# Optimization experiments

Measured on AMD Instinct MI355X. Metric: run time of the kernel, lower is better.

The kernel has to match this reference:

```python
import jax, jax.numpy as jnp
import numpy as np

C = 1024
RANK = 8


def _layernorm(x, g, b, eps=1e-5):
    mu = jnp.mean(x, axis=-1, keepdims=True)
    var = jnp.var(x, axis=-1, keepdims=True)
    return (x - mu) * jax.lax.rsqrt(var + eps) * g + b


def setup_inputs() -> dict:
    key = jax.random.key(0)
    ks = jax.random.split(key, 10)
    B, T = 4, 4096
    x = jax.random.normal(ks[0], (B, T, C), dtype=jnp.float32)
    # parameters (match torch inits)
    W0 = jnp.eye(C, dtype=jnp.float32) * 0.1
    A_init = jax.random.normal(ks[1], (C, RANK), dtype=jnp.float32) * 0.01
    B_init = jnp.zeros((RANK, C), dtype=jnp.float32)
    log_lr = jnp.full((C,), float(np.log(0.1)), dtype=jnp.float32)
    s = 1.0 / np.sqrt(C)
    Wq = jax.random.uniform(ks[2], (C, C), minval=-s, maxval=s, dtype=jnp.float32)
    Wk = jax.random.uniform(ks[3], (C, C), minval=-s, maxval=s, dtype=jnp.float32)
    Wv = jax.random.uniform(ks[4], (C, C), minval=-s, maxval=s, dtype=jnp.float32)
    Wo = jax.random.uniform(ks[5], (C, C), minval=-s, maxval=s, dtype=jnp.float32)
    Wg = jax.random.uniform(ks[6], (C, C), minval=-s, maxval=s, dtype=jnp.float32)
    ln_g = jnp.ones((C,), dtype=jnp.float32)
    ln_b = jnp.zeros((C,), dtype=jnp.float32)
    ls_g = jnp.full((C,), 1e-4, dtype=jnp.float32)  # LayerScale gamma
    return {"x": x, "W0": W0, "A_init": A_init, "B_init": B_init,
            "log_lr": log_lr, "Wq": Wq, "Wk": Wk, "Wv": Wv, "Wo": Wo,
            "Wg": Wg, "ln_g": ln_g, "ln_b": ln_b, "ls_g": ls_g}


def reference(x, W0, A_init, B_init, log_lr, Wq, Wk, Wv, Wo, Wg, ln_g, ln_b, ls_g):
    B, T, _ = x.shape
    h = _layernorm(x, ln_g, ln_b)
    # dual-form TTT (training path: q/k/v projections, full K @ W0)
    Q = jnp.einsum('btc,dc->btd', h, Wq)
    K = jnp.einsum('btc,dc->btd', h, Wk)
    V = jnp.einsum('btc,dc->btd', h, Wv)
    lr = jnp.minimum(jnp.exp(log_lr), 1.0)  # clamp(max=1.0)
    y0 = jnp.einsum('btc,cd->btd', K, W0) + jnp.einsum('btr,rd->btd', jnp.einsum('btc,cr->btr', K, A_init), B_init)
    error = y0 - V
    loss = jnp.mean(error ** 2)
    gradient = K * error                     # [B,T,C]
    grad_cumsum = jnp.cumsum(gradient, axis=1)
    grad_shift = jnp.concatenate([jnp.zeros((B, 1, gradient.shape[-1]), gradient.dtype), grad_cumsum[:, :-1, :]], axis=1)
    correction = Q * lr[None, None, :] * grad_shift
    pos = jnp.arange(1, T + 1, dtype=correction.dtype)
    pos_scale = (1.0 / (1.0 + 0.1 * jnp.log(pos)))[None, :, None]
    out = y0 - correction * pos_scale
    # gate, out projection, layer scale, residual
    gate = jax.nn.sigmoid(jnp.einsum('btc,dc->btd', x, Wg))
    out = out * gate
    out = jnp.einsum('btc,dc->btd', out, Wo) * ls_g
    return (x + out, loss)
```

## Files before the change

kernel.cpp:

```cpp
#include <hip/hip_runtime.h>
#include <stdint.h>
#include <math.h>

typedef unsigned short u16;
typedef __attribute__((ext_vector_type(8))) short short8;
typedef __attribute__((ext_vector_type(4))) float f32x4;

__device__ __forceinline__ float bf2f(u16 u){
  union { unsigned int i; float f; } v; v.i = ((unsigned int)u) << 16; return v.f;
}
__device__ __forceinline__ u16 f2bf(float f){
  union { float f; unsigned int i; } v; v.f = f;
  return (u16)((v.i + 0x7FFFu + ((v.i >> 16) & 1u)) >> 16);
}

__global__ void ln_prep(const float* __restrict__ x, const float* __restrict__ g,
                        const float* __restrict__ bta, u16* __restrict__ h,
                        u16* __restrict__ xb, float* __restrict__ loss){
  if (blockIdx.x == 0 && threadIdx.x == 0) loss[0] = 0.f;
  int row = blockIdx.x, tid = threadIdx.x;
  const float4* xr = (const float4*)(x + (size_t)row * 1024);
  float4 v = xr[tid];
  float s  = v.x + v.y + v.z + v.w;
  float s2 = v.x*v.x + v.y*v.y + v.z*v.z + v.w*v.w;
  #pragma unroll
  for (int o = 32; o > 0; o >>= 1){ s += __shfl_down(s, o); s2 += __shfl_down(s2, o); }
  __shared__ float red[8];
  if ((tid & 63) == 0){ red[tid >> 6] = s; red[4 + (tid >> 6)] = s2; }
  __syncthreads();
  float ts = red[0]+red[1]+red[2]+red[3];
  float t2 = red[4]+red[5]+red[6]+red[7];
  float mu   = ts * (1.0f/1024.0f);
  float var  = t2 * (1.0f/1024.0f) - mu*mu;
  float rstd = rsqrtf(var + 1e-5f);
  float4 gg = ((const float4*)g)[tid];
  float4 bb = ((const float4*)bta)[tid];
  ushort4 hv, xv;
  hv.x = f2bf((v.x-mu)*rstd*gg.x + bb.x);
  hv.y = f2bf((v.y-mu)*rstd*gg.y + bb.y);
  hv.z = f2bf((v.z-mu)*rstd*gg.z + bb.z);
  hv.w = f2bf((v.w-mu)*rstd*gg.w + bb.w);
  xv.x = f2bf(v.x); xv.y = f2bf(v.y); xv.z = f2bf(v.z); xv.w = f2bf(v.w);
  ((ushort4*)h )[(size_t)row*256 + tid] = hv;
  ((ushort4*)xb)[(size_t)row*256 + tid] = xv;
}

__global__ void conv5(const float* __restrict__ a, const float* __restrict__ b,
                      const float* __restrict__ c, const float* __restrict__ d,
                      const float* __restrict__ e,
                      u16* oa, u16* ob, u16* oc, u16* od, u16* oe){
  int sel = blockIdx.y;
  const float* s = sel==0?a : sel==1?b : sel==2?c : sel==3?d : e;
  u16* o = sel==0?oa : sel==1?ob : sel==2?oc : sel==3?od : oe;
  int i = blockIdx.x*256 + threadIdx.x;
  float4 v = ((const float4*)s)[i];
  ushort4 r; r.x=f2bf(v.x); r.y=f2bf(v.y); r.z=f2bf(v.z); r.w=f2bf(v.w);
  ((ushort4*)o)[i] = r;
}

__global__ void weff_k(const float* __restrict__ W0, const float* __restrict__ Ai,
                       const float* __restrict__ Bi, u16* __restrict__ Wet){
  __shared__ float tile[32][33];
  int d0 = blockIdx.x*32, e0 = blockIdx.y*32;
  int tid = threadIdx.x;
  int lr = tid >> 5, lc = tid & 31;
  #pragma unroll
  for (int s = 0; s < 4; ++s){
    int e = e0 + s*8 + lr, d = d0 + lc;
    float v = W0[(size_t)e*1024 + d];
    #pragma unroll
    for (int r = 0; r < 8; ++r) v += Ai[e*8 + r] * Bi[(size_t)r*1024 + d];
    tile[s*8 + lr][lc] = v;
  }
  __syncthreads();
  #pragma unroll
  for (int s = 0; s < 4; ++s){
    int d = d0 + s*8 + lr, e = e0 + lc;
    Wet[(size_t)d*1024 + e] = f2bf(tile[lc][s*8 + lr]);
  }
}

template<int EPI>
__device__ __forceinline__ void gemm_body(const u16* __restrict__ A, const u16* __restrict__ Bm,
    u16* __restrict__ Cb, float* __restrict__ Cf, const float* __restrict__ lsg,
    const float* __restrict__ xres, int mblk, int nblk){
  __shared__ u16 As[128*64];
  __shared__ u16 Bs[128*64];
  const int tid  = threadIdx.x;
  const int lane = tid & 63;
  const int w    = tid >> 6;
  const int m0 = mblk * 128, n0 = nblk * 128;
  const int lrow = lane >> 3, lcol8 = (lane & 7) * 8;
  const int wm = w & 1, wn = w >> 1;
  const int l15 = lane & 15, quad = lane >> 4;

  f32x4 acc[4][4] = {};

  #pragma unroll 1
  for (int kk = 0; kk < 1024; kk += 64){
    #pragma unroll
    for (int it = 0; it < 4; ++it){
      int r0 = w*8 + it*32;
      const u16* ga = A  + (size_t)(m0 + r0 + lrow)*1024 + kk + lcol8;
      __builtin_amdgcn_global_load_lds((const __attribute__((address_space(1))) unsigned int*)ga,
          (__attribute__((address_space(3))) unsigned int*)(As + r0*64), 16, 0, 0);
      const u16* gb = Bm + (size_t)(n0 + r0 + lrow)*1024 + kk + lcol8;
      __builtin_amdgcn_global_load_lds((const __attribute__((address_space(1))) unsigned int*)gb,
          (__attribute__((address_space(3))) unsigned int*)(Bs + r0*64), 16, 0, 0);
    }
    __syncthreads();
    #pragma unroll
    for (int kh = 0; kh < 2; ++kh){
      int kb = kh*32 + quad*8;
      short8 af[4], bfv[4];
      #pragma unroll
      for (int i = 0; i < 4; ++i) af[i]  = *(const short8*)(As + (wm*64 + i*16 + l15)*64 + kb);
      #pragma unroll
      for (int j = 0; j < 4; ++j) bfv[j] = *(const short8*)(Bs + (wn*64 + j*16 + l15)*64 + kb);
      #pragma unroll
      for (int i = 0; i < 4; ++i)
        #pragma unroll
        for (int j = 0; j < 4; ++j)
          acc[i][j] = __builtin_amdgcn_mfma_f32_16x16x32_bf16(af[i], bfv[j], acc[i][j], 0, 0, 0);
    }
    __syncthreads();
  }

  const int rbase = quad * 4;
  if (EPI == 0){
    #pragma unroll
    for (int i = 0; i < 4; ++i){
      int row = m0 + wm*64 + i*16 + rbase;
      #pragma unroll
      for (int j = 0; j < 4; ++j){
        int col = n0 + wn*64 + j*16 + l15;
        #pragma unroll
        for (int r = 0; r < 4; ++r)
          Cb[(size_t)(row + r)*1024 + col] = f2bf(acc[i][j][r]);
      }
    }
  } else {
    float lsv[4];
    #pragma unroll
    for (int j = 0; j < 4; ++j) lsv[j] = lsg[n0 + wn*64 + j*16 + l15];
    #pragma unroll
    for (int i = 0; i < 4; ++i){
      int row = m0 + wm*64 + i*16 + rbase;
      #pragma unroll
      for (int j = 0; j < 4; ++j){
        int col = n0 + wn*64 + j*16 + l15;
        #pragma unroll
        for (int r = 0; r < 4; ++r){
          size_t idx = (size_t)(row + r)*1024 + col;
          Cf[idx] = acc[i][j][r] * lsv[j] + xres[idx];
        }
      }
    }
  }
}

__global__ void gemm_qkvg(const u16* __restrict__ h, const u16* __restrict__ xb,
                          const u16* __restrict__ Wqb, const u16* __restrict__ Wkb,
                          const u16* __restrict__ Wvb, const u16* __restrict__ Wgb,
                          u16* __restrict__ Qb, u16* __restrict__ Kb,
                          u16* __restrict__ Vb, u16* __restrict__ Gb){
  int sel = blockIdx.y >> 3;
  const u16* A  = (sel == 3) ? xb : h;
  const u16* Bm = sel==0?Wqb : sel==1?Wkb : sel==2?Wvb : Wgb;
  u16* Out      = sel==0?Qb  : sel==1?Kb  : sel==2?Vb  : Gb;
  gemm_body<0>(A, Bm, Out, nullptr, nullptr, nullptr, blockIdx.x, blockIdx.y & 7);
}

__global__ void gemm_plain(const u16* __restrict__ A, const u16* __restrict__ Bm,
                           u16* __restrict__ C){
  gemm_body<0>(A, Bm, C, nullptr, nullptr, nullptr, blockIdx.x, blockIdx.y);
}

__global__ void gemm_final(const u16* __restrict__ A, const u16* __restrict__ Bm,
                           float* __restrict__ C, const float* __restrict__ lsg,
                           const float* __restrict__ xres){
  gemm_body<1>(A, Bm, nullptr, C, lsg, xres, blockIdx.x, blockIdx.y);
}

__global__ void scan1(const u16* __restrict__ Kb, const u16* __restrict__ Vb,
                      const u16* __restrict__ Yb, float* __restrict__ part,
                      float* __restrict__ loss){
  int tid = threadIdx.x;
  int c = blockIdx.x*256 + tid;
  int ch = blockIdx.y, b = blockIdx.z;
  size_t base = ((size_t)b*4096 + (size_t)ch*128)*1024 + c;
  float g = 0.f, ls = 0.f;
  #pragma unroll 8
  for (int t = 0; t < 128; ++t){
    size_t idx = base + (size_t)t*1024;
    float kv = bf2f(Kb[idx]), vv = bf2f(Vb[idx]), yv = bf2f(Yb[idx]);
    float e = yv - vv;
    g += kv*e; ls += e*e;
  }
  part[((size_t)(b*32 + ch))*1024 + c] = g;
  #pragma unroll
  for (int o = 32; o > 0; o >>= 1) ls += __shfl_down(ls, o);
  __shared__ float red[4];
  if ((tid & 63) == 0) red[tid >> 6] = ls;
  __syncthreads();
  if (tid == 0) atomicAdd(loss, red[0]+red[1]+red[2]+red[3]);
}

__global__ void scan2(const u16* __restrict__ Kb, const u16* __restrict__ Vb,
                      const u16* __restrict__ Yb, const u16* __restrict__ Qb,
                      const u16* __restrict__ Gb, const float* __restrict__ part,
                      const float* __restrict__ llr, u16* __restrict__ OutPre){
  int tid = threadIdx.x;
  int c = blockIdx.x*256 + tid;
  int ch = blockIdx.y, b = blockIdx.z;
  float run = 0.f;
  for (int j = 0; j < ch; ++j) run += part[((size_t)(b*32 + j))*1024 + c];
  float lrc = fminf(expf(llr[c]), 1.0f);
  size_t base = ((size_t)b*4096 + (size_t)ch*128)*1024 + c;
  #pragma unroll 4
  for (int t = 0; t < 128; ++t){
    size_t idx = base + (size_t)t*1024;
    float kv = bf2f(Kb[idx]), vv = bf2f(Vb[idx]), yv = bf2f(Yb[idx]);
    float qv = bf2f(Qb[idx]), gl = bf2f(Gb[idx]);
    float e = yv - vv;
    int tg = ch*128 + t + 1;
    float ps = 1.0f/(1.0f + 0.1f*logf((float)tg));
    float gate = 1.0f/(1.0f + expf(-gl));
    float o = (yv - qv*lrc*run*ps) * gate;
    OutPre[idx] = f2bf(o);
    run += kv*e;
  }
}

__global__ void finloss(const float* __restrict__ loss, float* __restrict__ o){
  o[0] = loss[0] * (1.0f/16777216.0f);
}

extern "C" void kernel_launch(void* const* d_in, const int* in_sizes, int n_in,
                              void* d_out, int out_size, void* d_ws, size_t ws_size,
                              hipStream_t stream){
  const float* x   = (const float*)d_in[0];
  const float* W0  = (const float*)d_in[1];
  const float* Ai  = (const float*)d_in[2];
  const float* Bi  = (const float*)d_in[3];
  const float* llr = (const float*)d_in[4];
  const float* Wq  = (const float*)d_in[5];
  const float* Wk  = (const float*)d_in[6];
  const float* Wv  = (const float*)d_in[7];
  const float* Wo  = (const float*)d_in[8];
  const float* Wg  = (const float*)d_in[9];
  const float* lng = (const float*)d_in[10];
  const float* lnb = (const float*)d_in[11];
  const float* lsg = (const float*)d_in[12];
  float* out = (float*)d_out;

  const size_t TOK = 16384, CC = 1024;
  char* p = (char*)d_ws;
  float* loss = (float*)p; p += 256;
  u16* h   = (u16*)p; p += TOK*CC*2;
  u16* xb  = (u16*)p; p += TOK*CC*2;
  u16* Qb  = (u16*)p; p += TOK*CC*2;
  u16* Kb  = (u16*)p; p += TOK*CC*2;
  u16* Vb  = (u16*)p; p += TOK*CC*2;
  u16* Gb  = (u16*)p; p += TOK*CC*2;
  u16* Wqb = (u16*)p; p += CC*CC*2;
  u16* Wkb = (u16*)p; p += CC*CC*2;
  u16* Wvb = (u16*)p; p += CC*CC*2;
  u16* Wgb = (u16*)p; p += CC*CC*2;
  u16* Wob = (u16*)p; p += CC*CC*2;
  u16* Wet = (u16*)p; p += CC*CC*2;
  float* part = (float*)p; p += (size_t)4*32*1024*4;

  ln_prep<<<16384, 256, 0, stream>>>(x, lng, lnb, h, xb, loss);
  conv5<<<dim3(1024, 5), 256, 0, stream>>>(Wq, Wk, Wv, Wg, Wo, Wqb, Wkb, Wvb, Wgb, Wob);
  weff_k<<<dim3(32, 32), 256, 0, stream>>>(W0, Ai, Bi, Wet);
  gemm_qkvg<<<dim3(128, 32), 256, 0, stream>>>(h, xb, Wqb, Wkb, Wvb, Wgb, Qb, Kb, Vb, Gb);
  gemm_plain<<<dim3(128, 8), 256, 0, stream>>>(Kb, Wet, h);
  scan1<<<dim3(4, 32, 4), 256, 0, stream>>>(Kb, Vb, h, part, loss);
  scan2<<<dim3(4, 32, 4), 256, 0, stream>>>(Kb, Vb, h, Qb, Gb, part, llr, Qb);
  gemm_final<<<dim3(128, 8), 256, 0, stream>>>(Qb, Wob, out, lsg, x);
  finloss<<<1, 1, 0, stream>>>(loss, out + 16777216);
}
```

Measured before the change: 468.8 us.

## Fuse gradient chunk-sum and loss into y0 GEMM epilogue; swizzle LDS tiles

```diff
diff --git a/kernel.cpp b/kernel.cpp
--- a/kernel.cpp
+++ b/kernel.cpp
@@ -83,16 +83,21 @@
 template<int EPI>
 __device__ __forceinline__ void gemm_body(const u16* __restrict__ A, const u16* __restrict__ Bm,
     u16* __restrict__ Cb, float* __restrict__ Cf, const float* __restrict__ lsg,
-    const float* __restrict__ xres, int mblk, int nblk){
+    const float* __restrict__ xres,
+    const u16* __restrict__ Kb2, const u16* __restrict__ Vb2,
+    u16* __restrict__ Gr, float* __restrict__ part, float* __restrict__ loss,
+    int mblk, int nblk){
   __shared__ u16 As[128*64];
   __shared__ u16 Bs[128*64];
   const int tid  = threadIdx.x;
   const int lane = tid & 63;
   const int w    = tid >> 6;
   const int m0 = mblk * 128, n0 = nblk * 128;
-  const int lrow = lane >> 3, lcol8 = (lane & 7) * 8;
+  const int lrow = lane >> 3;
+  const int gcol8 = (((lane & 7) ^ (lrow & 7)) * 8);
   const int wm = w & 1, wn = w >> 1;
   const int l15 = lane & 15, quad = lane >> 4;
+  const int sw  = (l15 & 7);
 
   f32x4 acc[4][4] = {};
 
@@ -101,22 +106,23 @@
     #pragma unroll
     for (int it = 0; it < 4; ++it){
       int r0 = w*8 + it*32;
-      const u16* ga = A  + (size_t)(m0 + r0 + lrow)*1024 + kk + lcol8;
+      const u16* ga = A  + (size_t)(m0 + r0 + lrow)*1024 + kk + gcol8;
       __builtin_amdgcn_global_load_lds((const __attribute__((address_space(1))) unsigned int*)ga,
           (__attribute__((address_space(3))) unsigned int*)(As + r0*64), 16, 0, 0);
-      const u16* gb = Bm + (size_t)(n0 + r0 + lrow)*1024 + kk + lcol8;
+      const u16* gb = Bm + (size_t)(n0 + r0 + lrow)*1024 + kk + gcol8;
       __builtin_amdgcn_global_load_lds((const __attribute__((address_space(1))) unsigned int*)gb,
           (__attribute__((address_space(3))) unsigned int*)(Bs + r0*64), 16, 0, 0);
     }
     __syncthreads();
     #pragma unroll
     for (int kh = 0; kh < 2; ++kh){
-      int kb = kh*32 + quad*8;
+      int kbi = kh*4 + quad;
+      int koff = ((kbi ^ sw) * 8);
       short8 af[4], bfv[4];
       #pragma unroll
-      for (int i = 0; i < 4; ++i) af[i]  = *(const short8*)(As + (wm*64 + i*16 + l15)*64 + kb);
-      #pragma unroll
-      for (int j = 0; j < 4; ++j) bfv[j] = *(const short8*)(Bs + (wn*64 + j*16 + l15)*64 + kb);
+      for (int i = 0; i < 4; ++i) af[i]  = *(const short8*)(As + (wm*64 + i*16 + l15)*64 + koff);
+      #pragma unroll
+      for (int j = 0; j < 4; ++j) bfv[j] = *(const short8*)(Bs + (wn*64 + j*16 + l15)*64 + koff);
       #pragma unroll
       for (int i = 0; i < 4; ++i)
         #pragma unroll
@@ -139,7 +145,7 @@
           Cb[(size_t)(row + r)*1024 + col] = f2bf(acc[i][j][r]);
       }
     }
-  } else {
+  } else if (EPI == 1){
     float lsv[4];
     #pragma unroll
     for (int j = 0; j < 4; ++j) lsv[j] = lsg[n0 + wn*64 + j*16 + l15];
@@ -156,6 +162,41 @@
         }
       }
     }
+  } else {
+    float csum[4] = {0.f, 0.f, 0.f, 0.f};
+    float ls = 0.f;
+    #pragma unroll
+    for (int i = 0; i < 4; ++i){
+      int row = m0 + wm*64 + i*16 + rbase;
+      #pragma unroll
+      for (int j = 0; j < 4; ++j){
+        int col = n0 + wn*64 + j*16 + l15;
+        #pragma unroll
+        for (int r = 0; r < 4; ++r){
+          size_t idx = (size_t)(row + r)*1024 + col;
+          float y  = acc[i][j][r];
+          float kv = bf2f(Kb2[idx]);
+          float vv = bf2f(Vb2[idx]);
+          float e  = y - vv;
+          float gv = kv * e;
+          Cb[idx] = f2bf(y);
+          Gr[idx] = f2bf(gv);
+          csum[j] += gv;
+          ls += e * e;
+        }
+      }
+    }
+    float* colred = (float*)As;
+    if (tid < 132) colred[tid] = 0.f;
+    __syncthreads();
+    #pragma unroll
+    for (int j = 0; j < 4; ++j) atomicAdd(&colred[wn*64 + j*16 + l15], csum[j]);
+    #pragma unroll
+    for (int o = 32; o > 0; o >>= 1) ls += __shfl_down(ls, o);
+    if (lane == 0) atomicAdd(&colred[128 + w], ls);
+    __syncthreads();
+    if (tid < 128) part[(size_t)mblk * 1024 + n0 + tid] = colred[tid];
+    if (tid == 0) atomicAdd(loss, colred[128]+colred[129]+colred[130]+colred[131]);
   }
 }
 
@@ -168,48 +209,29 @@
   const u16* A  = (sel == 3) ? xb : h;
   const u16* Bm = sel==0?Wqb : sel==1?Wkb : sel==2?Wvb : Wgb;
   u16* Out      = sel==0?Qb  : sel==1?Kb  : sel==2?Vb  : Gb;
-  gemm_body<0>(A, Bm, Out, nullptr, nullptr, nullptr, blockIdx.x, blockIdx.y & 7);
-}
-
-__global__ void gemm_plain(const u16* __restrict__ A, const u16* __restrict__ Bm,
-                           u16* __restrict__ C){
-  gemm_body<0>(A, Bm, C, nullptr, nullptr, nullptr, blockIdx.x, blockIdx.y);
+  gemm_body<0>(A, Bm, Out, nullptr, nullptr, nullptr,
+               nullptr, nullptr, nullptr, nullptr, nullptr, blockIdx.x, blockIdx.y & 7);
+}
+
+__global__ void gemm_y0(const u16* __restrict__ Kb, const u16* __restrict__ Wet,
+                        u16* __restrict__ Yb, const u16* __restrict__ Vb,
+                        u16* __restrict__ Gr, float* __restrict__ part,
+                        float* __restrict__ loss){
+  gemm_body<2>(Kb, Wet, Yb, nullptr, nullptr, nullptr,
+               Kb, Vb, Gr, part, loss, blockIdx.x, blockIdx.y);
 }
 
 __global__ void gemm_final(const u16* __restrict__ A, const u16* __restrict__ Bm,
                            float* __restrict__ C, const float* __restrict__ lsg,
                            const float* __restrict__ xres){
-  gemm_body<1>(A, Bm, nullptr, C, lsg, xres, blockIdx.x, blockIdx.y);
-}
-
-__global__ void scan1(const u16* __restrict__ Kb, const u16* __restrict__ Vb,
-                      const u16* __restrict__ Yb, float* __restrict__ part,
-                      float* __restrict__ loss){
-  int tid = threadIdx.x;
-  int c = blockIdx.x*256 + tid;
-  int ch = blockIdx.y, b = blockIdx.z;
-  size_t base = ((size_t)b*4096 + (size_t)ch*128)*1024 + c;
-  float g = 0.f, ls = 0.f;
-  #pragma unroll 8
-  for (int t = 0; t < 128; ++t){
-    size_t idx = base + (size_t)t*1024;
-    float kv = bf2f(Kb[idx]), vv = bf2f(Vb[idx]), yv = bf2f(Yb[idx]);
-    float e = yv - vv;
-    g += kv*e; ls += e*e;
-  }
-  part[((size_t)(b*32 + ch))*1024 + c] = g;
-  #pragma unroll
-  for (int o = 32; o > 0; o >>= 1) ls += __shfl_down(ls, o);
-  __shared__ float red[4];
-  if ((tid & 63) == 0) red[tid >> 6] = ls;
-  __syncthreads();
-  if (tid == 0) atomicAdd(loss, red[0]+red[1]+red[2]+red[3]);
-}
-
-__global__ void scan2(const u16* __restrict__ Kb, const u16* __restrict__ Vb,
-                      const u16* __restrict__ Yb, const u16* __restrict__ Qb,
-                      const u16* __restrict__ Gb, const float* __restrict__ part,
-                      const float* __restrict__ llr, u16* __restrict__ OutPre){
+  gemm_body<1>(A, Bm, nullptr, C, lsg, xres,
+               nullptr, nullptr, nullptr, nullptr, nullptr, blockIdx.x, blockIdx.y);
+}
+
+__global__ void scan2(const u16* __restrict__ Gr, const u16* __restrict__ Yb,
+                      const u16* __restrict__ Qb, const u16* __restrict__ Gb,
+                      const float* __restrict__ part, const float* __restrict__ llr,
+                      u16* __restrict__ OutPre){
   int tid = threadIdx.x;
   int c = blockIdx.x*256 + tid;
   int ch = blockIdx.y, b = blockIdx.z;
@@ -220,15 +242,16 @@
   #pragma unroll 4
   for (int t = 0; t < 128; ++t){
     size_t idx = base + (size_t)t*1024;
-    float kv = bf2f(Kb[idx]), vv = bf2f(Vb[idx]), yv = bf2f(Yb[idx]);
-    float qv = bf2f(Qb[idx]), gl = bf2f(Gb[idx]);
-    float e = yv - vv;
+    float gr = bf2f(Gr[idx]);
+    float yv = bf2f(Yb[idx]);
+    float qv = bf2f(Qb[idx]);
+    float gl = bf2f(Gb[idx]);
     int tg = ch*128 + t + 1;
     float ps = 1.0f/(1.0f + 0.1f*logf((float)tg));
     float gate = 1.0f/(1.0f + expf(-gl));
     float o = (yv - qv*lrc*run*ps) * gate;
     OutPre[idx] = f2bf(o);
-    run += kv*e;
+    run += gr;
   }
 }
 
@@ -269,15 +292,14 @@
   u16* Wgb = (u16*)p; p += CC*CC*2;
   u16* Wob = (u16*)p; p += CC*CC*2;
   u16* Wet = (u16*)p; p += CC*CC*2;
-  float* part = (float*)p; p += (size_t)4*32*1024*4;
+  float* part = (float*)p; p += (size_t)128*1024*4;
 
   ln_prep<<<16384, 256, 0, stream>>>(x, lng, lnb, h, xb, loss);
   conv5<<<dim3(1024, 5), 256, 0, stream>>>(Wq, Wk, Wv, Wg, Wo, Wqb, Wkb, Wvb, Wgb, Wob);
   weff_k<<<dim3(32, 32), 256, 0, stream>>>(W0, Ai, Bi, Wet);
   gemm_qkvg<<<dim3(128, 32), 256, 0, stream>>>(h, xb, Wqb, Wkb, Wvb, Wgb, Qb, Kb, Vb, Gb);
-  gemm_plain<<<dim3(128, 8), 256, 0, stream>>>(Kb, Wet, h);
-  scan1<<<dim3(4, 32, 4), 256, 0, stream>>>(Kb, Vb, h, part, loss);
-  scan2<<<dim3(4, 32, 4), 256, 0, stream>>>(Kb, Vb, h, Qb, Gb, part, llr, Qb);
+  gemm_y0<<<dim3(128, 8), 256, 0, stream>>>(Kb, Wet, h, Vb, xb, part, loss);
+  scan2<<<dim3(4, 32, 4), 256, 0, stream>>>(xb, h, Qb, Gb, part, llr, Qb);
   gemm_final<<<dim3(128, 8), 256, 0, stream>>>(Qb, Wob, out, lsg, x);
   finloss<<<1, 1, 0, stream>>>(loss, out + 16777216);
 }
```

Measured after the change: 500.6 us. +6.8%, slower.
